# Kernel optimization log

Measured on AMD Instinct MI355X. Metric: run time of the kernel, lower is better.

## Reference

```python
import jax, jax.numpy as jnp
import numpy as np

N, L, S, H, D = 2, 2048, 2048, 8, 64

def elu_feature_map(x):
    return jax.nn.elu(x) + 1.0

def setup_inputs() -> dict:
    key = jax.random.key(0)
    k1, k2, k3, k4, k5 = jax.random.split(key, 5)
    return {
        "queries": jax.random.normal(k1, (N, L, H, D), dtype=jnp.float32),
        "keys": jax.random.normal(k2, (N, S, H, D), dtype=jnp.float32),
        "values": jax.random.normal(k3, (N, S, H, D), dtype=jnp.float32),
        "q_mask": jnp.ones((N, L), dtype=jnp.float32),
        "kv_mask": jnp.ones((N, S), dtype=jnp.float32),
        "W": jax.random.normal(k4, (1, 2), dtype=jnp.float32) * 0.5,  # nn.Linear(2,1) weight
        "b": jax.random.normal(k5, (1,), dtype=jnp.float32) * 0.5,    # nn.Linear(2,1) bias
    }

def reference(queries, keys, values, q_mask, kv_mask, W, b):
    # feature map: elu(x) + 1
    Q = elu_feature_map(queries) * q_mask[:, :, None, None]   # [N,L,H,D]
    K = elu_feature_map(keys) * kv_mask[:, :, None, None]     # [N,S,H,D]
    queries_m = queries * q_mask[:, :, None, None]
    values_m = values * kv_mask[:, :, None, None]  # masked but unused downstream (as in original)
    del values_m
    # full QK score tensor [N,L,S,H]
    qk = jnp.einsum('nlhd,nshd->nlsh', Q, K)
    qk_mean = jnp.mean(qk, axis=2)  # [N,L,H]
    qk_max = jnp.max(qk, axis=2)    # [N,L,H]
    stats = jnp.stack([qk_mean, qk_max], axis=-1)  # [N,L,H,2]
    gate = jax.nn.sigmoid(jnp.einsum('nlhe,oe->nlho', stats, W) + b)  # [N,L,H,1]
    atten = gate[..., 0]  # [N,L,H]
    return queries_m * atten[..., None]  # [N,L,H,D]
```

## Files before the change

kernel.cpp:

```cpp
#include <hip/hip_runtime.h>
#include <math.h>

#define N_ 2
#define L_ 2048
#define S_ 2048
#define H_ 8
#define D_ 64

#define BLK_L 256
#define BS 64
#define SSPLIT 4
#define TILES (S_ / SSPLIT / BS)
#define KPAD 72
#define KP 16

typedef __attribute__((ext_vector_type(8))) short short8;
typedef __attribute__((ext_vector_type(4))) float floatx4;

__device__ __forceinline__ float feat(float x) {
    return x > 0.0f ? x + 1.0f : __expf(x);
}
__device__ __forceinline__ short f2bf(float x) {
    unsigned u = __float_as_uint(x);
    unsigned r = (u + 0x7fffu + ((u >> 16) & 1u)) >> 16;
    return (short)r;
}
__device__ __forceinline__ float bf2f(short h) {
    return __uint_as_float(((unsigned)(unsigned short)h) << 16);
}

__global__ __launch_bounds__(256) void ksum_kernel(const float* __restrict__ K,
        const float* __restrict__ kvmask, float* __restrict__ Kpart) {
    int nh = blockIdx.x;
    int z = blockIdx.y;
    int n = nh >> 3, h = nh & 7;
    int t = threadIdx.x;
    int d = t & 63, sc = t >> 6;
    float sum = 0.f;
    int s0 = z * (S_ / KP) + sc * 32;
    #pragma unroll 4
    for (int k = 0; k < 32; ++k) {
        int s = s0 + k;
        float v = K[(((size_t)n * S_ + s) * H_ + h) * D_ + d];
        sum += feat(v) * kvmask[n * S_ + s];
    }
    __shared__ float sm[256];
    sm[t] = sum;
    __syncthreads();
    if (t < 64) {
        Kpart[(z * 16 + nh) * 64 + t] =
            sm[t] + sm[t + 64] + sm[t + 128] + sm[t + 192];
    }
}

__global__ __launch_bounds__(256) void rowmax_mfma(
        const float* __restrict__ Q, const float* __restrict__ K,
        const float* __restrict__ qmask, const float* __restrict__ kvmask,
        float* __restrict__ rowpart) {
    __shared__ short Kh[2][BS * KPAD];
    __shared__ short Kl[2][BS * KPAD];

    int nh = blockIdx.y;
    int n = nh >> 3, h = nh & 7;
    int t = threadIdx.x;
    int w = t >> 6, lane = t & 63;
    int quad = lane >> 4, l16 = lane & 15;
    int lblock = blockIdx.x * BLK_L;
    int z = blockIdx.z;

    short8 Ah[4][2], Al[4][2];
    #pragma unroll
    for (int lsub = 0; lsub < 4; ++lsub) {
        int lrow = lblock + w * 64 + lsub * 16 + l16;
        float qm = qmask[n * L_ + lrow];
        const float* qp = Q + (((size_t)n * L_ + lrow) * H_ + h) * D_ + quad * 8;
        #pragma unroll
        for (int ks = 0; ks < 2; ++ks) {
            float4 v0 = *(const float4*)(qp + ks * 32);
            float4 v1 = *(const float4*)(qp + ks * 32 + 4);
            float fv[8];
            fv[0] = feat(v0.x) * qm; fv[1] = feat(v0.y) * qm;
            fv[2] = feat(v0.z) * qm; fv[3] = feat(v0.w) * qm;
            fv[4] = feat(v1.x) * qm; fv[5] = feat(v1.y) * qm;
            fv[6] = feat(v1.z) * qm; fv[7] = feat(v1.w) * qm;
            short8 hi, lo;
            #pragma unroll
            for (int j = 0; j < 8; ++j) {
                short hb = f2bf(fv[j]);
                hi[j] = hb;
                lo[j] = f2bf(fv[j] - bf2f(hb));
            }
            Ah[lsub][ks] = hi;
            Al[lsub][ks] = lo;
        }
    }

    int srow = t >> 2, chunk = t & 3;
    float4 sv[4];
    float skm;

    auto loadreg = [&](int tile) {
        int sbase = z * (S_ / SSPLIT) + tile * BS;
        const float* kp = K + (((size_t)n * S_ + sbase + srow) * H_ + h) * D_ + chunk * 16;
        sv[0] = *(const float4*)(kp);
        sv[1] = *(const float4*)(kp + 4);
        sv[2] = *(const float4*)(kp + 8);
        sv[3] = *(const float4*)(kp + 12);
        skm = kvmask[n * S_ + sbase + srow];
    };
    auto storelds = [&](int buf) {
        float fv[16];
        #pragma unroll
        for (int j = 0; j < 4; ++j) {
            fv[4 * j + 0] = feat(sv[j].x) * skm;
            fv[4 * j + 1] = feat(sv[j].y) * skm;
            fv[4 * j + 2] = feat(sv[j].z) * skm;
            fv[4 * j + 3] = feat(sv[j].w) * skm;
        }
        short8 h0, h1, l0, l1;
        #pragma unroll
        for (int j = 0; j < 8; ++j) {
            short hb = f2bf(fv[j]);
            h0[j] = hb;
            l0[j] = f2bf(fv[j] - bf2f(hb));
            short hb2 = f2bf(fv[8 + j]);
            h1[j] = hb2;
            l1[j] = f2bf(fv[8 + j] - bf2f(hb2));
        }
        short* dh = &Kh[buf][srow * KPAD + chunk * 16];
        short* dl = &Kl[buf][srow * KPAD + chunk * 16];
        *(short8*)(dh)     = h0;
        *(short8*)(dh + 8) = h1;
        *(short8*)(dl)     = l0;
        *(short8*)(dl + 8) = l1;
    };

    float rmax[4][4];
    #pragma unroll
    for (int i = 0; i < 4; ++i)
        #pragma unroll
        for (int r = 0; r < 4; ++r) rmax[i][r] = 0.f;

    loadreg(0);
    storelds(0);
    __syncthreads();

    for (int tile = 0; tile < TILES; ++tile) {
        int cur = tile & 1;
        if (tile + 1 < TILES) loadreg(tile + 1);

        #pragma unroll
        for (int ssub = 0; ssub < 4; ++ssub) {
            const short* bph = &Kh[cur][(ssub * 16 + l16) * KPAD + quad * 8];
            const short* bpl = &Kl[cur][(ssub * 16 + l16) * KPAD + quad * 8];
            short8 Bh0 = *(const short8*)(bph);
            short8 Bh1 = *(const short8*)(bph + 32);
            short8 Bl0 = *(const short8*)(bpl);
            short8 Bl1 = *(const short8*)(bpl + 32);
            #pragma unroll
            for (int lsub = 0; lsub < 4; ++lsub) {
                floatx4 acc = {0.f, 0.f, 0.f, 0.f};
                acc = __builtin_amdgcn_mfma_f32_16x16x32_bf16(Ah[lsub][0], Bh0, acc, 0, 0, 0);
                acc = __builtin_amdgcn_mfma_f32_16x16x32_bf16(Ah[lsub][1], Bh1, acc, 0, 0, 0);
                acc = __builtin_amdgcn_mfma_f32_16x16x32_bf16(Ah[lsub][0], Bl0, acc, 0, 0, 0);
                acc = __builtin_amdgcn_mfma_f32_16x16x32_bf16(Ah[lsub][1], Bl1, acc, 0, 0, 0);
                acc = __builtin_amdgcn_mfma_f32_16x16x32_bf16(Al[lsub][0], Bh0, acc, 0, 0, 0);
                acc = __builtin_amdgcn_mfma_f32_16x16x32_bf16(Al[lsub][1], Bh1, acc, 0, 0, 0);
                #pragma unroll
                for (int r = 0; r < 4; ++r)
                    rmax[lsub][r] = fmaxf(rmax[lsub][r], acc[r]);
            }
        }

        if (tile + 1 < TILES) storelds(1 - cur);
        __syncthreads();
    }

    #pragma unroll
    for (int lsub = 0; lsub < 4; ++lsub)
        #pragma unroll
        for (int r = 0; r < 4; ++r) {
            float m = rmax[lsub][r];
            m = fmaxf(m, __shfl_xor(m, 1, 64));
            m = fmaxf(m, __shfl_xor(m, 2, 64));
            m = fmaxf(m, __shfl_xor(m, 4, 64));
            m = fmaxf(m, __shfl_xor(m, 8, 64));
            if (l16 == 0) {
                int l = lblock + w * 64 + lsub * 16 + quad * 4 + r;
                rowpart[((size_t)z * 16 + nh) * L_ + l] = m;
            }
        }
}

__global__ __launch_bounds__(256) void finalize_kernel(
        const float* __restrict__ Q, const float* __restrict__ qmask,
        const float* __restrict__ Kpart, const float* __restrict__ rowpart,
        const float* __restrict__ W, const float* __restrict__ b,
        float* __restrict__ out) {
    int nh = blockIdx.y;
    int n = nh >> 3, h = nh & 7;
    int lblock = blockIdx.x * 64;
    int t = threadIdx.x;
    int w = t >> 6, lane = t & 63;

    float ks = 0.f;
    #pragma unroll
    for (int p = 0; p < KP; ++p)
        ks += Kpart[(p * 16 + nh) * 64 + lane];

    float w0 = W[0], w1 = W[1], bb = b[0];

    #pragma unroll 4
    for (int r = 0; r < 16; ++r) {
        int l = lblock + w * 16 + r;
        float q = Q[(((size_t)n * L_ + l) * H_ + h) * D_ + lane];
        float qm = qmask[n * L_ + l];
        float p = feat(q) * qm * ks;
        #pragma unroll
        for (int off = 32; off > 0; off >>= 1)
            p += __shfl_xor(p, off, 64);
        float mx = 0.f;
        #pragma unroll
        for (int zz = 0; zz < SSPLIT; ++zz)
            mx = fmaxf(mx, rowpart[((size_t)zz * 16 + nh) * L_ + l]);
        float g = 1.0f / (1.0f + __expf(-(w0 * p * (1.0f / S_) + w1 * mx + bb)));
        out[(((size_t)n * L_ + l) * H_ + h) * D_ + lane] = q * qm * g;
    }
}

extern "C" void kernel_launch(void* const* d_in, const int* in_sizes, int n_in,
                              void* d_out, int out_size, void* d_ws, size_t ws_size,
                              hipStream_t stream) {
    const float* Q      = (const float*)d_in[0];
    const float* K      = (const float*)d_in[1];
    const float* qmask  = (const float*)d_in[3];
    const float* kvmask = (const float*)d_in[4];
    const float* W      = (const float*)d_in[5];
    const float* b      = (const float*)d_in[6];
    float* out = (float*)d_out;

    float* Kpart   = (float*)d_ws;
    float* rowpart = (float*)d_ws + KP * 16 * 64;

    ksum_kernel<<<dim3(N_ * H_, KP), 256, 0, stream>>>(K, kvmask, Kpart);
    rowmax_mfma<<<dim3(L_ / BLK_L, N_ * H_, SSPLIT), 256, 0, stream>>>(
        Q, K, qmask, kvmask, rowpart);
    finalize_kernel<<<dim3(L_ / 64, N_ * H_), 256, 0, stream>>>(
        Q, qmask, Kpart, rowpart, W, b, out);
}
```

Before: 132.3 us.

## Precompute split-bf16 K features once and double S split for rowmax

```diff
diff --git a/kernel.cpp b/kernel.cpp
--- a/kernel.cpp
+++ b/kernel.cpp
@@ -9,12 +9,13 @@
 
 #define BLK_L 256
 #define BS 64
-#define SSPLIT 4
+#define SSPLIT 8
 #define TILES (S_ / SSPLIT / BS)
-#define KPAD 72
-#define KP 16
+#define KROW 80
+#define KP 32
 
 typedef __attribute__((ext_vector_type(8))) short short8;
+typedef __attribute__((ext_vector_type(4))) short short4v;
 typedef __attribute__((ext_vector_type(4))) float floatx4;
 
 __device__ __forceinline__ float feat(float x) {
@@ -29,36 +30,51 @@
     return __uint_as_float(((unsigned)(unsigned short)h) << 16);
 }
 
-__global__ __launch_bounds__(256) void ksum_kernel(const float* __restrict__ K,
-        const float* __restrict__ kvmask, float* __restrict__ Kpart) {
+__global__ __launch_bounds__(256) void kprep_kernel(const float* __restrict__ K,
+        const float* __restrict__ kvmask, short* __restrict__ KH,
+        short* __restrict__ KL, float* __restrict__ Kpart) {
     int nh = blockIdx.x;
-    int z = blockIdx.y;
+    int sc = blockIdx.y;
     int n = nh >> 3, h = nh & 7;
     int t = threadIdx.x;
-    int d = t & 63, sc = t >> 6;
-    float sum = 0.f;
-    int s0 = z * (S_ / KP) + sc * 32;
-    #pragma unroll 4
-    for (int k = 0; k < 32; ++k) {
-        int s = s0 + k;
-        float v = K[(((size_t)n * S_ + s) * H_ + h) * D_ + d];
-        sum += feat(v) * kvmask[n * S_ + s];
-    }
-    __shared__ float sm[256];
-    sm[t] = sum;
+    int sr = t >> 4;
+    int d4 = (t & 15) * 4;
+    float sums[4] = {0.f, 0.f, 0.f, 0.f};
+    #pragma unroll
+    for (int p = 0; p < 4; ++p) {
+        int s = sc * 64 + p * 16 + sr;
+        float km = kvmask[n * S_ + s];
+        float4 v = *(const float4*)(K + (((size_t)n * S_ + s) * H_ + h) * D_ + d4);
+        float f0 = feat(v.x) * km, f1 = feat(v.y) * km;
+        float f2 = feat(v.z) * km, f3 = feat(v.w) * km;
+        sums[0] += f0; sums[1] += f1; sums[2] += f2; sums[3] += f3;
+        short4v hi, lo;
+        hi.x = f2bf(f0); lo.x = f2bf(f0 - bf2f(hi.x));
+        hi.y = f2bf(f1); lo.y = f2bf(f1 - bf2f(hi.y));
+        hi.z = f2bf(f2); lo.z = f2bf(f2 - bf2f(hi.z));
+        hi.w = f2bf(f3); lo.w = f2bf(f3 - bf2f(hi.w));
+        size_t o = ((size_t)nh * S_ + s) * 64 + d4;
+        *(short4v*)(KH + o) = hi;
+        *(short4v*)(KL + o) = lo;
+    }
+    __shared__ float smf[16][64];
+    #pragma unroll
+    for (int j = 0; j < 4; ++j) smf[sr][d4 + j] = sums[j];
     __syncthreads();
     if (t < 64) {
-        Kpart[(z * 16 + nh) * 64 + t] =
-            sm[t] + sm[t + 64] + sm[t + 128] + sm[t + 192];
-    }
-}
-
-__global__ __launch_bounds__(256) void rowmax_mfma(
-        const float* __restrict__ Q, const float* __restrict__ K,
-        const float* __restrict__ qmask, const float* __restrict__ kvmask,
+        float s = 0.f;
+        #pragma unroll
+        for (int r = 0; r < 16; ++r) s += smf[r][t];
+        Kpart[(sc * 16 + nh) * 64 + t] = s;
+    }
+}
+
+__global__ __launch_bounds__(256, 4) void rowmax_mfma(
+        const float* __restrict__ Q, const short* __restrict__ KH,
+        const short* __restrict__ KL, const float* __restrict__ qmask,
         float* __restrict__ rowpart) {
-    __shared__ short Kh[2][BS * KPAD];
-    __shared__ short Kl[2][BS * KPAD];
+    __shared__ short Kh[2][BS * KROW];
+    __shared__ short Kl[2][BS * KROW];
 
     int nh = blockIdx.y;
     int n = nh >> 3, h = nh & 7;
@@ -95,44 +111,26 @@
         }
     }
 
-    int srow = t >> 2, chunk = t & 3;
-    float4 sv[4];
-    float skm;
-
+    short8 svh[2], svl[2];
     auto loadreg = [&](int tile) {
         int sbase = z * (S_ / SSPLIT) + tile * BS;
-        const float* kp = K + (((size_t)n * S_ + sbase + srow) * H_ + h) * D_ + chunk * 16;
-        sv[0] = *(const float4*)(kp);
-        sv[1] = *(const float4*)(kp + 4);
-        sv[2] = *(const float4*)(kp + 8);
-        sv[3] = *(const float4*)(kp + 12);
-        skm = kvmask[n * S_ + sbase + srow];
+        #pragma unroll
+        for (int p = 0; p < 2; ++p) {
+            int id = t + 256 * p;
+            int s = id >> 3, g = id & 7;
+            size_t o = ((size_t)nh * S_ + sbase + s) * 64 + g * 8;
+            svh[p] = *(const short8*)(KH + o);
+            svl[p] = *(const short8*)(KL + o);
+        }
     };
     auto storelds = [&](int buf) {
-        float fv[16];
-        #pragma unroll
-        for (int j = 0; j < 4; ++j) {
-            fv[4 * j + 0] = feat(sv[j].x) * skm;
-            fv[4 * j + 1] = feat(sv[j].y) * skm;
-            fv[4 * j + 2] = feat(sv[j].z) * skm;
-            fv[4 * j + 3] = feat(sv[j].w) * skm;
-        }
-        short8 h0, h1, l0, l1;
-        #pragma unroll
-        for (int j = 0; j < 8; ++j) {
-            short hb = f2bf(fv[j]);
-            h0[j] = hb;
-            l0[j] = f2bf(fv[j] - bf2f(hb));
-            short hb2 = f2bf(fv[8 + j]);
-            h1[j] = hb2;
-            l1[j] = f2bf(fv[8 + j] - bf2f(hb2));
-        }
-        short* dh = &Kh[buf][srow * KPAD + chunk * 16];
-        short* dl = &Kl[buf][srow * KPAD + chunk * 16];
-        *(short8*)(dh)     = h0;
-        *(short8*)(dh + 8) = h1;
-        *(short8*)(dl)     = l0;
-        *(short8*)(dl + 8) = l1;
+        #pragma unroll
+        for (int p = 0; p < 2; ++p) {
+            int id = t + 256 * p;
+            int s = id >> 3, g = id & 7;
+            *(short8*)(&Kh[buf][s * KROW + g * 8]) = svh[p];
+            *(short8*)(&Kl[buf][s * KROW + g * 8]) = svl[p];
+        }
     };
 
     float rmax[4][4];
@@ -151,8 +149,8 @@
 
         #pragma unroll
         for (int ssub = 0; ssub < 4; ++ssub) {
-            const short* bph = &Kh[cur][(ssub * 16 + l16) * KPAD + quad * 8];
-            const short* bpl = &Kl[cur][(ssub * 16 + l16) * KPAD + quad * 8];
+            const short* bph = &Kh[cur][(ssub * 16 + l16) * KROW + quad * 8];
+            const short* bpl = &Kl[cur][(ssub * 16 + l16) * KROW + quad * 8];
             short8 Bh0 = *(const short8*)(bph);
             short8 Bh1 = *(const short8*)(bph + 32);
             short8 Bl0 = *(const short8*)(bpl);
@@ -204,7 +202,7 @@
     int w = t >> 6, lane = t & 63;
 
     float ks = 0.f;
-    #pragma unroll
+    #pragma unroll 8
     for (int p = 0; p < KP; ++p)
         ks += Kpart[(p * 16 + nh) * 64 + lane];
 
@@ -239,12 +237,15 @@
     const float* b      = (const float*)d_in[6];
     float* out = (float*)d_out;
 
-    float* Kpart   = (float*)d_ws;
-    float* rowpart = (float*)d_ws + KP * 16 * 64;
-
-    ksum_kernel<<<dim3(N_ * H_, KP), 256, 0, stream>>>(K, kvmask, Kpart);
+    char* ws = (char*)d_ws;
+    float* Kpart   = (float*)(ws);
+    float* rowpart = (float*)(ws + 131072);
+    short* KH      = (short*)(ws + 131072 + 1048576);
+    short* KL      = (short*)(ws + 131072 + 1048576 + 4194304);
+
+    kprep_kernel<<<dim3(N_ * H_, S_ / 64), 256, 0, stream>>>(K, kvmask, KH, KL, Kpart);
     rowmax_mfma<<<dim3(L_ / BLK_L, N_ * H_, SSPLIT), 256, 0, stream>>>(
-        Q, K, qmask, kvmask, rowpart);
+        Q, KH, KL, qmask, rowpart);
     finalize_kernel<<<dim3(L_ / 64, N_ * H_), 256, 0, stream>>>(
         Q, qmask, Kpart, rowpart, W, b, out);
 }
```

Result: slower. 173.6 us (+31.2%).

## Double S-split, flatten grid with z-fastest order, vectorize K-sum, repad LDS

Applied to the files above, without the earlier changes.

```diff
diff --git a/kernel.cpp b/kernel.cpp
--- a/kernel.cpp
+++ b/kernel.cpp
@@ -9,10 +9,10 @@
 
 #define BLK_L 256
 #define BS 64
-#define SSPLIT 4
+#define SSPLIT 8
 #define TILES (S_ / SSPLIT / BS)
-#define KPAD 72
-#define KP 16
+#define KROW 80
+#define KP 32
 
 typedef __attribute__((ext_vector_type(8))) short short8;
 typedef __attribute__((ext_vector_type(4))) float floatx4;
@@ -32,41 +32,49 @@
 __global__ __launch_bounds__(256) void ksum_kernel(const float* __restrict__ K,
         const float* __restrict__ kvmask, float* __restrict__ Kpart) {
     int nh = blockIdx.x;
-    int z = blockIdx.y;
+    int sc = blockIdx.y;
     int n = nh >> 3, h = nh & 7;
     int t = threadIdx.x;
-    int d = t & 63, sc = t >> 6;
-    float sum = 0.f;
-    int s0 = z * (S_ / KP) + sc * 32;
-    #pragma unroll 4
-    for (int k = 0; k < 32; ++k) {
-        int s = s0 + k;
-        float v = K[(((size_t)n * S_ + s) * H_ + h) * D_ + d];
-        sum += feat(v) * kvmask[n * S_ + s];
-    }
-    __shared__ float sm[256];
-    sm[t] = sum;
+    int sr = t >> 4;
+    int d4 = (t & 15) * 4;
+    float sums[4] = {0.f, 0.f, 0.f, 0.f};
+    #pragma unroll
+    for (int p = 0; p < 4; ++p) {
+        int s = sc * 64 + p * 16 + sr;
+        float km = kvmask[n * S_ + s];
+        float4 v = *(const float4*)(K + (((size_t)n * S_ + s) * H_ + h) * D_ + d4);
+        sums[0] += feat(v.x) * km; sums[1] += feat(v.y) * km;
+        sums[2] += feat(v.z) * km; sums[3] += feat(v.w) * km;
+    }
+    __shared__ float smf[16][64];
+    #pragma unroll
+    for (int j = 0; j < 4; ++j) smf[sr][d4 + j] = sums[j];
     __syncthreads();
     if (t < 64) {
-        Kpart[(z * 16 + nh) * 64 + t] =
-            sm[t] + sm[t + 64] + sm[t + 128] + sm[t + 192];
-    }
-}
-
-__global__ __launch_bounds__(256) void rowmax_mfma(
+        float s = 0.f;
+        #pragma unroll
+        for (int r = 0; r < 16; ++r) s += smf[r][t];
+        Kpart[(sc * 16 + nh) * 64 + t] = s;
+    }
+}
+
+__global__ __launch_bounds__(256, 4) void rowmax_mfma(
         const float* __restrict__ Q, const float* __restrict__ K,
         const float* __restrict__ qmask, const float* __restrict__ kvmask,
         float* __restrict__ rowpart) {
-    __shared__ short Kh[2][BS * KPAD];
-    __shared__ short Kl[2][BS * KPAD];
-
-    int nh = blockIdx.y;
+    __shared__ short Kh[2][BS * KROW];
+    __shared__ short Kl[2][BS * KROW];
+
+    int bid = blockIdx.x;
+    int ltile = bid >> 7;
+    int rem = bid & 127;
+    int nh = rem >> 3;
+    int z = rem & 7;
     int n = nh >> 3, h = nh & 7;
     int t = threadIdx.x;
     int w = t >> 6, lane = t & 63;
     int quad = lane >> 4, l16 = lane & 15;
-    int lblock = blockIdx.x * BLK_L;
-    int z = blockIdx.z;
+    int lblock = ltile * BLK_L;
 
     short8 Ah[4][2], Al[4][2];
     #pragma unroll
@@ -108,7 +116,7 @@
         sv[3] = *(const float4*)(kp + 12);
         skm = kvmask[n * S_ + sbase + srow];
     };
-    auto storelds = [&](int buf) {
+    auto featstore = [&](int buf) {
         float fv[16];
         #pragma unroll
         for (int j = 0; j < 4; ++j) {
@@ -127,8 +135,8 @@
             h1[j] = hb2;
             l1[j] = f2bf(fv[8 + j] - bf2f(hb2));
         }
-        short* dh = &Kh[buf][srow * KPAD + chunk * 16];
-        short* dl = &Kl[buf][srow * KPAD + chunk * 16];
+        short* dh = &Kh[buf][srow * KROW + chunk * 16];
+        short* dl = &Kl[buf][srow * KROW + chunk * 16];
         *(short8*)(dh)     = h0;
         *(short8*)(dh + 8) = h1;
         *(short8*)(dl)     = l0;
@@ -142,7 +150,7 @@
         for (int r = 0; r < 4; ++r) rmax[i][r] = 0.f;
 
     loadreg(0);
-    storelds(0);
+    featstore(0);
     __syncthreads();
 
     for (int tile = 0; tile < TILES; ++tile) {
@@ -151,8 +159,8 @@
 
         #pragma unroll
         for (int ssub = 0; ssub < 4; ++ssub) {
-            const short* bph = &Kh[cur][(ssub * 16 + l16) * KPAD + quad * 8];
-            const short* bpl = &Kl[cur][(ssub * 16 + l16) * KPAD + quad * 8];
+            const short* bph = &Kh[cur][(ssub * 16 + l16) * KROW + quad * 8];
+            const short* bpl = &Kl[cur][(ssub * 16 + l16) * KROW + quad * 8];
             short8 Bh0 = *(const short8*)(bph);
             short8 Bh1 = *(const short8*)(bph + 32);
             short8 Bl0 = *(const short8*)(bpl);
@@ -172,7 +180,7 @@
             }
         }
 
-        if (tile + 1 < TILES) storelds(1 - cur);
+        if (tile + 1 < TILES) featstore(1 - cur);
         __syncthreads();
     }
 
@@ -204,7 +212,7 @@
     int w = t >> 6, lane = t & 63;
 
     float ks = 0.f;
-    #pragma unroll
+    #pragma unroll 8
     for (int p = 0; p < KP; ++p)
         ks += Kpart[(p * 16 + nh) * 64 + lane];
 
@@ -242,8 +250,8 @@
     float* Kpart   = (float*)d_ws;
     float* rowpart = (float*)d_ws + KP * 16 * 64;
 
-    ksum_kernel<<<dim3(N_ * H_, KP), 256, 0, stream>>>(K, kvmask, Kpart);
-    rowmax_mfma<<<dim3(L_ / BLK_L, N_ * H_, SSPLIT), 256, 0, stream>>>(
+    ksum_kernel<<<dim3(N_ * H_, S_ / 64), 256, 0, stream>>>(K, kvmask, Kpart);
+    rowmax_mfma<<<dim3((L_ / BLK_L) * (N_ * H_) * SSPLIT), 256, 0, stream>>>(
         Q, K, qmask, kvmask, rowpart);
     finalize_kernel<<<dim3(L_ / 64, N_ * H_), 256, 0, stream>>>(
         Q, qmask, Kpart, rowpart, W, b, out);
```

Measured after the change: 175.9 us. 33.0% more time.
